# Optimization experiments

Measured on AMD Instinct MI355X. Metric: run time of the kernel, lower is better.

Reference implementation:

```python
import jax, jax.numpy as jnp
import numpy as np

EPS = 1e-08

def rms_norm(x, eps=EPS):
    # Matches torch: mean-centered, population variance (unbiased=False)
    mean = jnp.mean(x, axis=-1, keepdims=True)
    var = jnp.var(x, axis=-1, keepdims=True)
    return (x - mean) / jnp.sqrt(var + eps)

def activation_quant(x):
    s = 127.0 / jnp.max(jnp.abs(x), axis=-1, keepdims=True)
    return jnp.clip(jnp.round(s * x), -128, 127) / s

def ternary_matmul(x, w):
    # pos_mask - neg_mask of sign(w) equals sign(w); x @ sign(w).T
    return jnp.matmul(x, jnp.sign(w).T)

def setup_inputs() -> dict:
    key = jax.random.key(0)
    k0, k1, k2, k3 = jax.random.split(key, 4)
    B, S, D, H = 4, 2048, 2048, 8192
    x = jax.random.normal(k0, (B, S, D), dtype=jnp.float32)
    W_g = jax.random.normal(k1, (H, D), dtype=jnp.float32) * 0.01
    W_u = jax.random.normal(k2, (H, D), dtype=jnp.float32) * 0.01
    W_d = jax.random.normal(k3, (D, H), dtype=jnp.float32) * 0.01
    return {"x": x, "W_g": W_g, "W_u": W_u, "W_d": W_d}

def reference(x, W_g, W_u, W_d):
    xq = activation_quant(rms_norm(x))
    g = jax.nn.silu(ternary_matmul(xq, W_g))   # [B,S,H]
    u = ternary_matmul(xq, W_u)                # [B,S,H]
    p = g * u
    return ternary_matmul(p, W_d)              # [B,S,D]
```

## Files before the change

kernel.cpp:

```cpp
#include <hip/hip_runtime.h>
#include <stdint.h>

#define MROWS 8192
#define DDIM  2048
#define HDIM  8192

typedef __attribute__((ext_vector_type(8))) short bf16x8;
typedef __attribute__((ext_vector_type(4))) float f32x4;
typedef __attribute__((ext_vector_type(4))) int   i32x4;
typedef unsigned short u16;

__device__ __forceinline__ void async_load16(const void* g, void* l) {
  auto gp = reinterpret_cast<const __attribute__((address_space(1))) unsigned int*>(
      reinterpret_cast<uintptr_t>(g));
  auto lp = reinterpret_cast<__attribute__((address_space(3))) unsigned int*>(
      reinterpret_cast<uintptr_t>(l));
  __builtin_amdgcn_global_load_lds(gp, lp, 16, 0, 0);
}

__device__ __forceinline__ u16 f2bf(float f) {
  union { float f; unsigned int u; } v; v.f = f;
  unsigned int r = v.u + 0x7FFF + ((v.u >> 16) & 1);
  return (u16)(r >> 16);
}

__global__ void sign_i8x2_kernel(const float* __restrict__ wg, const float* __restrict__ wu,
                                 char* __restrict__ og, char* __restrict__ ou) {
  const int t = blockIdx.x * 256 + threadIdx.x;
  const float* w = blockIdx.y ? wu : wg;
  char* o = blockIdx.y ? ou : og;
  const float4* w4 = (const float4*)w;
  float4 a = w4[t * 2], b = w4[t * 2 + 1];
  float v[8] = {a.x, a.y, a.z, a.w, b.x, b.y, b.z, b.w};
  union { char s[8]; uint2 u; } pk;
#pragma unroll
  for (int i = 0; i < 8; i++)
    pk.s[i] = v[i] > 0.f ? (char)1 : (v[i] < 0.f ? (char)-1 : (char)0);
  ((uint2*)o)[t] = pk.u;
}

__global__ void sign_bf16_kernel(const float* __restrict__ w, u16* __restrict__ o) {
  const int t = blockIdx.x * 256 + threadIdx.x;
  const float4* w4 = (const float4*)w;
  float4 a = w4[t * 2], b = w4[t * 2 + 1];
  float v[8] = {a.x, a.y, a.z, a.w, b.x, b.y, b.z, b.w};
  union { u16 s[8]; uint4 u; } pk;
#pragma unroll
  for (int i = 0; i < 8; i++)
    pk.s[i] = v[i] > 0.f ? 0x3F80 : (v[i] < 0.f ? 0xBF80 : 0);
  ((uint4*)o)[t] = pk.u;
}

__global__ void norm_quant_i8_kernel(const float* __restrict__ x,
                                     char* __restrict__ q, float* __restrict__ inv) {
  const int row  = blockIdx.x;
  const int tid  = threadIdx.x;
  const int lane = tid & 63, wave = tid >> 6;
  const float4* xr = (const float4*)(x + (size_t)row * DDIM);
  float4 a = xr[tid * 2], b = xr[tid * 2 + 1];
  float v[8] = {a.x, a.y, a.z, a.w, b.x, b.y, b.z, b.w};
  float s1 = 0.f, s2 = 0.f;
#pragma unroll
  for (int i = 0; i < 8; i++) { s1 += v[i]; s2 += v[i] * v[i]; }
#pragma unroll
  for (int o = 1; o < 64; o <<= 1) { s1 += __shfl_xor(s1, o); s2 += __shfl_xor(s2, o); }
  __shared__ float ssum[4], ssq[4], smax[4];
  if (lane == 0) { ssum[wave] = s1; ssq[wave] = s2; }
  __syncthreads();
  s1 = ssum[0] + ssum[1] + ssum[2] + ssum[3];
  s2 = ssq[0] + ssq[1] + ssq[2] + ssq[3];
  const float mean = s1 * (1.f / DDIM);
  const float var  = s2 * (1.f / DDIM) - mean * mean;
  const float rstd = rsqrtf(var + 1e-8f);
  float mx = 0.f;
#pragma unroll
  for (int i = 0; i < 8; i++) { v[i] = (v[i] - mean) * rstd; mx = fmaxf(mx, fabsf(v[i])); }
#pragma unroll
  for (int o = 1; o < 64; o <<= 1) mx = fmaxf(mx, __shfl_xor(mx, o));
  if (lane == 0) smax[wave] = mx;
  __syncthreads();
  mx = fmaxf(fmaxf(smax[0], smax[1]), fmaxf(smax[2], smax[3]));
  const float s = 127.f / mx;
  if (tid == 0) inv[row] = mx * (1.f / 127.f);
  union { char s8[8]; uint2 u; } pk;
#pragma unroll
  for (int i = 0; i < 8; i++) {
    float qq = rintf(v[i] * s);
    qq = fminf(fmaxf(qq, -128.f), 127.f);
    pk.s8[i] = (char)(int)qq;
  }
  ((uint2*)(q + (size_t)row * DDIM))[tid] = pk.u;
}

__global__ __launch_bounds__(512, 2) void gemm_glu_i8_kernel(
    const char* __restrict__ A,
    const char* __restrict__ Bg,
    const char* __restrict__ Bu,
    const float* __restrict__ inv,
    u16* __restrict__ P)
{
  constexpr int K  = DDIM;
  constexpr int NT = K / 128;
  const int l   = blockIdx.x + gridDim.x * blockIdx.y;
  const int xcd = l & 7;
  const int s_  = l >> 3;
  const int n0 = (xcd * 8 + (s_ & 7)) * 128;
  const int m0 = (s_ >> 3) * 256;
  const int tid  = threadIdx.x;
  const int lane = tid & 63, wave = tid >> 6;
  const int wm = wave >> 1, wn = wave & 1;
  const int quad = lane >> 4, l16 = lane & 15;

  __shared__ __align__(16) char lds[131072];

  i32x4 accg[4][4], accu[4][4];
  const i32x4 zero = {0, 0, 0, 0};
#pragma unroll
  for (int i = 0; i < 4; i++)
#pragma unroll
    for (int j = 0; j < 4; j++) { accg[i][j] = zero; accu[i][j] = zero; }

  const int arow = wm * 64 + l16;
  const int brow = wn * 64 + l16;
  const int swz  = (l16 & 7) << 4;

  const int rr  = tid >> 3;
  const int cbs = ((tid & 7) << 4) ^ ((rr & 7) << 4);
  const char* aSrc = A  + (size_t)(m0 + rr) * K + cbs;
  const char* gSrc = Bg + (size_t)(n0 + rr) * K + cbs;
  const char* uSrc = Bu + (size_t)(n0 + rr) * K + cbs;

#define STG_A(is) async_load16(aSrc + (size_t)(is) * 64 * K + k0n, bufN + (is) * 8192 + wave * 1024)
#define STG_G(is) async_load16(gSrc + (size_t)(is) * 64 * K + k0n, bufN + 32768 + (is) * 8192 + wave * 1024)
#define STG_U(is) async_load16(uSrc + (size_t)(is) * 64 * K + k0n, bufN + 49152 + (is) * 8192 + wave * 1024)

  {
    char* bufN = lds;
    const int k0n = 0;
    STG_A(0); STG_A(1); STG_A(2); STG_A(3);
    STG_G(0); STG_G(1); STG_U(0); STG_U(1);
    asm volatile("s_waitcnt vmcnt(0)" ::: "memory");
    __builtin_amdgcn_s_barrier();
  }

  for (int t = 0; t < NT; ++t) {
    const char* bufC = lds + (size_t)(t & 1) * 65536;
    char* bufN = lds + (size_t)((t + 1) & 1) * 65536;
    const int k0n = (t + 1) * 128;
    const bool pre = (t + 1) < NT;
    i32x4 a[4];
#pragma unroll
    for (int ks = 0; ks < 2; ++ks) {
#pragma unroll
      for (int jh = 0; jh < 2; ++jh) {
        const int koff = (ks * 64 + quad * 16) ^ swz;
        if (jh == 0) {
#pragma unroll
          for (int i = 0; i < 4; ++i)
            a[i] = *(const i32x4*)(bufC + (size_t)(arow + i * 16) * 128 + koff);
        }
        i32x4 bg[2], bu[2];
#pragma unroll
        for (int jj = 0; jj < 2; ++jj) {
          const int j = jh * 2 + jj;
          bg[jj] = *(const i32x4*)(bufC + 32768 + (size_t)(brow + j * 16) * 128 + koff);
          bu[jj] = *(const i32x4*)(bufC + 49152 + (size_t)(brow + j * 16) * 128 + koff);
        }
        const int ph = ks * 2 + jh;
        if (pre) {
          if (ph == 0)      { STG_A(0); STG_A(1); STG_A(2); }
          else if (ph == 1) { STG_A(3); STG_G(0); STG_G(1); }
          else if (ph == 2) { STG_U(0); STG_U(1); }
        }
        __builtin_amdgcn_s_barrier();
        asm volatile("s_waitcnt lgkmcnt(0)" ::: "memory");
        __builtin_amdgcn_s_setprio(1);
#pragma unroll
        for (int i = 0; i < 4; ++i)
#pragma unroll
          for (int jj = 0; jj < 2; ++jj) {
            const int j = jh * 2 + jj;
            accg[i][j] = __builtin_amdgcn_mfma_i32_16x16x64_i8(a[i], bg[jj], accg[i][j], 0, 0, 0);
            accu[i][j] = __builtin_amdgcn_mfma_i32_16x16x64_i8(a[i], bu[jj], accu[i][j], 0, 0, 0);
          }
        __builtin_amdgcn_s_setprio(0);
        if (ph == 3) asm volatile("s_waitcnt vmcnt(0)" ::: "memory");
        __builtin_amdgcn_s_barrier();
      }
    }
  }
#undef STG_A
#undef STG_G
#undef STG_U

  const int rbase = m0 + wm * 64 + quad * 4;
  const int cbase = n0 + wn * 64 + l16;
#pragma unroll
  for (int i = 0; i < 4; i++) {
    float iv[4];
#pragma unroll
    for (int r = 0; r < 4; r++) iv[r] = inv[rbase + i * 16 + r];
#pragma unroll
    for (int j = 0; j < 4; j++)
#pragma unroll
      for (int r = 0; r < 4; r++) {
        float g = (float)accg[i][j][r] * iv[r];
        float u = (float)accu[i][j][r] * iv[r];
        float pv = (g / (1.f + __expf(-g))) * u;
        P[(size_t)(rbase + i * 16 + r) * HDIM + (cbase + j * 16)] = f2bf(pv);
      }
  }
}

__global__ __launch_bounds__(512, 2) void gemm_out_kernel(
    const u16* __restrict__ A,
    const u16* __restrict__ B,
    float* __restrict__ C)
{
  constexpr size_t KB = (size_t)HDIM * 2;
  constexpr int NT = (int)(KB / 128);
  const int l   = blockIdx.x + gridDim.x * blockIdx.y;
  const int xcd = l & 7;
  const int s_  = l >> 3;
  const int n0 = xcd * 256;
  const int m0 = s_ * 256;
  const int tid  = threadIdx.x;
  const int lane = tid & 63, wave = tid >> 6;
  const int wm = wave >> 2, wn = wave & 3;
  const int quad = lane >> 4, l16 = lane & 15;

  __shared__ __align__(16) char lds[131072];

  f32x4 acc[8][4];
  const f32x4 zero = {0.f, 0.f, 0.f, 0.f};
#pragma unroll
  for (int i = 0; i < 8; i++)
#pragma unroll
    for (int j = 0; j < 4; j++) acc[i][j] = zero;

  const int arow = wm * 128 + l16;
  const int brow = wn * 64 + l16;
  const int swz  = (l16 & 7) << 4;

  const int rr  = tid >> 3;
  const int cbs = ((tid & 7) << 4) ^ ((rr & 7) << 4);
  const char* aSrc = (const char*)A + (size_t)(m0 + rr) * KB + cbs;
  const char* bSrc = (const char*)B + (size_t)(n0 + rr) * KB + cbs;

#define STG2_A(is) async_load16(aSrc + (size_t)(is) * 64 * KB + k0n, bufN + (is) * 8192 + wave * 1024)
#define STG2_B(is) async_load16(bSrc + (size_t)(is) * 64 * KB + k0n, bufN + 32768 + (is) * 8192 + wave * 1024)

  {
    char* bufN = lds;
    const int k0n = 0;
    STG2_A(0); STG2_A(1); STG2_A(2); STG2_A(3);
    STG2_B(0); STG2_B(1); STG2_B(2); STG2_B(3);
    asm volatile("s_waitcnt vmcnt(0)" ::: "memory");
    __builtin_amdgcn_s_barrier();
  }

  for (int t = 0; t < NT; ++t) {
    const char* bufC = lds + (size_t)(t & 1) * 65536;
    char* bufN = lds + (size_t)((t + 1) & 1) * 65536;
    const int k0n = (t + 1) * 128;
    const bool pre = (t + 1) < NT;
    bf16x8 b[4];
#pragma unroll
    for (int ks = 0; ks < 2; ++ks) {
#pragma unroll
      for (int ih = 0; ih < 2; ++ih) {
        const int koff = (ks * 64 + quad * 16) ^ swz;
        if (ih == 0) {
#pragma unroll
          for (int j = 0; j < 4; ++j)
            b[j] = *(const bf16x8*)(bufC + 32768 + (size_t)(brow + j * 16) * 128 + koff);
        }
        bf16x8 a[4];
#pragma unroll
        for (int ii = 0; ii < 4; ++ii)
          a[ii] = *(const bf16x8*)(bufC + (size_t)(arow + (ih * 4 + ii) * 16) * 128 + koff);
        const int ph = ks * 2 + ih;
        if (pre) {
          if (ph == 0)      { STG2_A(0); STG2_A(1); STG2_A(2); }
          else if (ph == 1) { STG2_A(3); STG2_B(0); STG2_B(1); }
          else if (ph == 2) { STG2_B(2); STG2_B(3); }
        }
        __builtin_amdgcn_s_barrier();
        asm volatile("s_waitcnt lgkmcnt(0)" ::: "memory");
        __builtin_amdgcn_s_setprio(1);
#pragma unroll
        for (int ii = 0; ii < 4; ++ii) {
          const int i = ih * 4 + ii;
#pragma unroll
          for (int j = 0; j < 4; ++j)
            acc[i][j] = __builtin_amdgcn_mfma_f32_16x16x32_bf16(a[ii], b[j], acc[i][j], 0, 0, 0);
        }
        __builtin_amdgcn_s_setprio(0);
        if (ph == 3) asm volatile("s_waitcnt vmcnt(0)" ::: "memory");
        __builtin_amdgcn_s_barrier();
      }
    }
  }
#undef STG2_A
#undef STG2_B

  const int rbase = m0 + wm * 128 + quad * 4;
  const int cbase = n0 + wn * 64 + l16;
#pragma unroll
  for (int i = 0; i < 8; i++)
#pragma unroll
    for (int j = 0; j < 4; j++)
#pragma unroll
      for (int r = 0; r < 4; r++)
        C[(size_t)(rbase + i * 16 + r) * DDIM + (cbase + j * 16)] = acc[i][j][r];
}

extern "C" void kernel_launch(void* const* d_in, const int* in_sizes, int n_in,
                              void* d_out, int out_size, void* d_ws, size_t ws_size,
                              hipStream_t stream) {
  const float* x  = (const float*)d_in[0];
  const float* Wg = (const float*)d_in[1];
  const float* Wu = (const float*)d_in[2];
  const float* Wd = (const float*)d_in[3];

  char* ws = (char*)d_ws;
  char*  q    = ws;
  float* inv  = (float*)(ws + 16777216ull);
  char*  sWg  = ws + 20971520ull;
  char*  sWu  = ws + 37748736ull;
  u16*   sWd  = (u16*)(ws + 54525952ull);
  u16*   p    = (u16*)(ws + 88080384ull);
  float* out  = (float*)d_out;

  dim3 gs(8192, 2);
  sign_i8x2_kernel<<<gs, 256, 0, stream>>>(Wg, Wu, sWg, sWu);
  sign_bf16_kernel<<<8192, 256, 0, stream>>>(Wd, sWd);

  norm_quant_i8_kernel<<<MROWS, 256, 0, stream>>>(x, q, inv);

  dim3 g1(HDIM / 128, MROWS / 256);
  gemm_glu_i8_kernel<<<g1, 512, 0, stream>>>(q, sWg, sWu, inv, p);

  dim3 g2(DDIM / 256, MROWS / 256);
  gemm_out_kernel<<<g2, 512, 0, stream>>>(p, sWd, out);
}
```

Measured before the change: 785.4 us.

## Prefetch two K-tiles ahead and move LDS refill to end of iteration

Both GEMM kernels now issue global-to-LDS loads two K-tiles ahead instead of one, still using the two LDS buffers. The per-phase staged prefetches and per-phase barriers are replaced by one full-tile refill after each tile's compute, with a vmcnt(8) wait so one tile's loads stay in flight. This is meant to hide global memory latency and cut barriers per iteration. In exchange, loads no longer overlap with compute inside the same tile, the lgkmcnt wait before the MFMAs is removed, and refilling the just-consumed buffer needs correct barrier ordering.

```diff
diff --git a/kernel.cpp b/kernel.cpp
--- a/kernel.cpp
+++ b/kernel.cpp
@@ -133,21 +133,22 @@
 #define STG_A(is) async_load16(aSrc + (size_t)(is) * 64 * K + k0n, bufN + (is) * 8192 + wave * 1024)
 #define STG_G(is) async_load16(gSrc + (size_t)(is) * 64 * K + k0n, bufN + 32768 + (is) * 8192 + wave * 1024)
 #define STG_U(is) async_load16(uSrc + (size_t)(is) * 64 * K + k0n, bufN + 49152 + (is) * 8192 + wave * 1024)
+#define STG_TILE() do { STG_A(0); STG_A(1); STG_A(2); STG_A(3); \
+                        STG_G(0); STG_G(1); STG_U(0); STG_U(1); } while (0)
 
   {
-    char* bufN = lds;
-    const int k0n = 0;
-    STG_A(0); STG_A(1); STG_A(2); STG_A(3);
-    STG_G(0); STG_G(1); STG_U(0); STG_U(1);
-    asm volatile("s_waitcnt vmcnt(0)" ::: "memory");
-    __builtin_amdgcn_s_barrier();
-  }
+    char* bufN = lds;           const int k0n = 0;
+    STG_TILE();
+  }
+  {
+    char* bufN = lds + 65536;   const int k0n = 128;
+    STG_TILE();
+  }
+  asm volatile("s_waitcnt vmcnt(8)" ::: "memory");
+  __builtin_amdgcn_s_barrier();
 
   for (int t = 0; t < NT; ++t) {
     const char* bufC = lds + (size_t)(t & 1) * 65536;
-    char* bufN = lds + (size_t)((t + 1) & 1) * 65536;
-    const int k0n = (t + 1) * 128;
-    const bool pre = (t + 1) < NT;
     i32x4 a[4];
 #pragma unroll
     for (int ks = 0; ks < 2; ++ks) {
@@ -166,14 +167,7 @@
           bg[jj] = *(const i32x4*)(bufC + 32768 + (size_t)(brow + j * 16) * 128 + koff);
           bu[jj] = *(const i32x4*)(bufC + 49152 + (size_t)(brow + j * 16) * 128 + koff);
         }
-        const int ph = ks * 2 + jh;
-        if (pre) {
-          if (ph == 0)      { STG_A(0); STG_A(1); STG_A(2); }
-          else if (ph == 1) { STG_A(3); STG_G(0); STG_G(1); }
-          else if (ph == 2) { STG_U(0); STG_U(1); }
-        }
         __builtin_amdgcn_s_barrier();
-        asm volatile("s_waitcnt lgkmcnt(0)" ::: "memory");
         __builtin_amdgcn_s_setprio(1);
 #pragma unroll
         for (int i = 0; i < 4; ++i)
@@ -184,14 +178,23 @@
             accu[i][j] = __builtin_amdgcn_mfma_i32_16x16x64_i8(a[i], bu[jj], accu[i][j], 0, 0, 0);
           }
         __builtin_amdgcn_s_setprio(0);
-        if (ph == 3) asm volatile("s_waitcnt vmcnt(0)" ::: "memory");
-        __builtin_amdgcn_s_barrier();
       }
     }
+    __builtin_amdgcn_s_barrier();
+    if (t + 2 < NT) {
+      char* bufN = lds + (size_t)(t & 1) * 65536;
+      const int k0n = (t + 2) * 128;
+      STG_TILE();
+      asm volatile("s_waitcnt vmcnt(8)" ::: "memory");
+    } else {
+      asm volatile("s_waitcnt vmcnt(0)" ::: "memory");
+    }
+    __builtin_amdgcn_s_barrier();
   }
 #undef STG_A
 #undef STG_G
 #undef STG_U
+#undef STG_TILE
 
   const int rbase = m0 + wm * 64 + quad * 4;
   const int cbase = n0 + wn * 64 + l16;
@@ -249,21 +252,22 @@
 
 #define STG2_A(is) async_load16(aSrc + (size_t)(is) * 64 * KB + k0n, bufN + (is) * 8192 + wave * 1024)
 #define STG2_B(is) async_load16(bSrc + (size_t)(is) * 64 * KB + k0n, bufN + 32768 + (is) * 8192 + wave * 1024)
+#define STG2_TILE() do { STG2_A(0); STG2_A(1); STG2_A(2); STG2_A(3); \
+                         STG2_B(0); STG2_B(1); STG2_B(2); STG2_B(3); } while (0)
 
   {
-    char* bufN = lds;
-    const int k0n = 0;
-    STG2_A(0); STG2_A(1); STG2_A(2); STG2_A(3);
-    STG2_B(0); STG2_B(1); STG2_B(2); STG2_B(3);
-    asm volatile("s_waitcnt vmcnt(0)" ::: "memory");
-    __builtin_amdgcn_s_barrier();
-  }
+    char* bufN = lds;           const int k0n = 0;
+    STG2_TILE();
+  }
+  {
+    char* bufN = lds + 65536;   const int k0n = 128;
+    STG2_TILE();
+  }
+  asm volatile("s_waitcnt vmcnt(8)" ::: "memory");
+  __builtin_amdgcn_s_barrier();
 
   for (int t = 0; t < NT; ++t) {
     const char* bufC = lds + (size_t)(t & 1) * 65536;
-    char* bufN = lds + (size_t)((t + 1) & 1) * 65536;
-    const int k0n = (t + 1) * 128;
-    const bool pre = (t + 1) < NT;
     bf16x8 b[4];
 #pragma unroll
     for (int ks = 0; ks < 2; ++ks) {
@@ -279,14 +283,7 @@
 #pragma unroll
         for (int ii = 0; ii < 4; ++ii)
           a[ii] = *(const bf16x8*)(bufC + (size_t)(arow + (ih * 4 + ii) * 16) * 128 + koff);
-        const int ph = ks * 2 + ih;
-        if (pre) {
-          if (ph == 0)      { STG2_A(0); STG2_A(1); STG2_A(2); }
-          else if (ph == 1) { STG2_A(3); STG2_B(0); STG2_B(1); }
-          else if (ph == 2) { STG2_B(2); STG2_B(3); }
-        }
         __builtin_amdgcn_s_barrier();
-        asm volatile("s_waitcnt lgkmcnt(0)" ::: "memory");
         __builtin_amdgcn_s_setprio(1);
 #pragma unroll
         for (int ii = 0; ii < 4; ++ii) {
@@ -296,13 +293,22 @@
             acc[i][j] = __builtin_amdgcn_mfma_f32_16x16x32_bf16(a[ii], b[j], acc[i][j], 0, 0, 0);
         }
         __builtin_amdgcn_s_setprio(0);
-        if (ph == 3) asm volatile("s_waitcnt vmcnt(0)" ::: "memory");
-        __builtin_amdgcn_s_barrier();
       }
     }
+    __builtin_amdgcn_s_barrier();
+    if (t + 2 < NT) {
+      char* bufN = lds + (size_t)(t & 1) * 65536;
+      const int k0n = (t + 2) * 128;
+      STG2_TILE();
+      asm volatile("s_waitcnt vmcnt(8)" ::: "memory");
+    } else {
+      asm volatile("s_waitcnt vmcnt(0)" ::: "memory");
+    }
+    __builtin_amdgcn_s_barrier();
   }
 #undef STG2_A
 #undef STG2_B
+#undef STG2_TILE
 
   const int rbase = m0 + wm * 128 + quad * 4;
   const int cbase = n0 + wn * 64 + l16;
```

New measurement: 759.9 us. -3.2%, faster.
